# Performance work log

Hardware: AMD Instinct MI355X
Metric: run time of the kernel (lower is better)

Reference implementation:

```python
import jax, jax.numpy as jnp
import numpy as np

TEMPERATURE = 0.5
W_WITHIN = 1.0
W_CROSS = 0.5
MARGIN = 0.1


def setup_inputs() -> dict:
    key = jax.random.key(0)
    k1, k2 = jax.random.split(key)
    features = jax.random.normal(k1, (8192, 256), dtype=jnp.float32)
    gene_labels = jax.random.randint(k2, (8192,), 0, 200, dtype=jnp.int64 if jax.config.jax_enable_x64 else jnp.int32)
    return {"features": features, "gene_labels": gene_labels}


def reference(features, gene_labels):
    B = features.shape[0]
    # L2-normalize rows, full pairwise cosine similarity / temperature
    fn = features / jnp.linalg.norm(features, axis=1, keepdims=True)
    sim = (fn @ fn.T) / TEMPERATURE  # [B, B]

    same = gene_labels[:, None] == gene_labels[None, :]  # [B, B]
    eye = jnp.eye(B, dtype=bool)
    same_off = same & ~eye            # same-gene, off-diagonal (gene_similarity)
    neg = ~same                       # different-gene pairs (cross_gene_mask)
    has_neg = neg.any(axis=1)

    # Per-anchor logsumexp over negatives (sim of anchor i to all different-gene samples)
    neg_sim = jnp.where(neg, sim, -jnp.inf)
    lse_neg = jax.scipy.special.logsumexp(neg_sim, axis=1)
    lse_neg = jnp.where(has_neg, lse_neg, 0.0)  # rows with no negatives are masked out below

    # Within-gene loss: for each unordered same-gene pair (i<j) with gene != -1 and
    # anchor i having >=1 negative: CE([sim_ij, neg_sims_i], label=0)
    #   = -sim_ij + logaddexp(sim_ij, lse_neg_i) = softplus(lse_neg_i - sim_ij)
    upper = jnp.triu(jnp.ones((B, B), dtype=bool), k=1)
    valid_gene = (gene_labels != -1)[:, None]
    pair_mask = same_off & upper & valid_gene & has_neg[:, None]
    within_gene_loss = jnp.where(pair_mask, jax.nn.softplus(lse_neg[:, None] - sim), 0.0).sum()

    # Cross-gene loss: mean over all ordered different-gene pairs of relu(sim - margin)
    cross_cnt = neg.sum()
    cross_sum = jnp.where(neg, jax.nn.relu(sim - MARGIN), 0.0).sum()
    cross_gene_loss = jnp.where(cross_cnt > 0, cross_sum / jnp.maximum(cross_cnt, 1).astype(sim.dtype), 0.0)

    total_loss = W_WITHIN * within_gene_loss + W_CROSS * cross_gene_loss
    num_within_gene_pairs = same_off.sum().astype(sim.dtype)
    num_cross_gene_pairs = cross_cnt
    return total_loss, within_gene_loss, cross_gene_loss, num_within_gene_pairs, num_cross_gene_pairs
```

## Files before the change

kernel.cpp:

```cpp
#include <hip/hip_runtime.h>
#include <math.h>

#define B_N   8192
#define D_K   256
#define NGENE 200
#define MAXN  512

typedef short  bf16x8 __attribute__((ext_vector_type(8)));
typedef float  f32x4  __attribute__((ext_vector_type(4)));

#define OFF_FNBF    0u
#define OFF_LPART   4194304u
#define OFF_HIST    4718592u
#define OFF_OFFS    4719616u
#define OFF_SORTED  4720640u
#define OFF_CROSSP  4753408u
#define OFF_WITHINP 4755456u
#define OFF_CCORR   4756480u

__device__ __forceinline__ unsigned short f2bf(float f) {
    unsigned int u = __float_as_uint(f);
    unsigned int r = u + 0x7fffu + ((u >> 16) & 1u);
    return (unsigned short)(r >> 16);
}
__device__ __forceinline__ float bf2f_lo(unsigned int u) { return __uint_as_float(u << 16); }
__device__ __forceinline__ float bf2f_hi(unsigned int u) { return __uint_as_float(u & 0xffff0000u); }

__global__ __launch_bounds__(256) void k_np(const float* __restrict__ feat,
                                            const int* __restrict__ lab,
                                            unsigned short* __restrict__ fnbf,
                                            int* __restrict__ hist,
                                            int* __restrict__ offs,
                                            int* __restrict__ sorted) {
    if (blockIdx.x < 2048) {
        int wave = threadIdx.x >> 6, lane = threadIdx.x & 63;
        int row  = blockIdx.x * 4 + wave;
        const float4* src = reinterpret_cast<const float4*>(feat + (size_t)row * D_K);
        float4 v = src[lane];
        float ss = v.x * v.x + v.y * v.y + v.z * v.z + v.w * v.w;
#pragma unroll
        for (int m = 1; m < 64; m <<= 1) ss += __shfl_xor(ss, m);
        float rn = 1.0f / sqrtf(ss);
        ushort4 o;
        o.x = f2bf(v.x * rn); o.y = f2bf(v.y * rn);
        o.z = f2bf(v.z * rn); o.w = f2bf(v.w * rn);
        reinterpret_cast<ushort4*>(fnbf + (size_t)row * D_K)[lane] = o;
        return;
    }
    __shared__ int sh_hist[256], sh_scan[256], sh_cur[256];
    int t = threadIdx.x;
    sh_hist[t] = 0;
    __syncthreads();
    for (int i = t; i < B_N; i += 256) {
        int lb = lab[i];
        if (lb >= 0 && lb < NGENE) atomicAdd(&sh_hist[lb], 1);
    }
    __syncthreads();
    int v = sh_hist[t];
    sh_scan[t] = v;
    __syncthreads();
#pragma unroll
    for (int d = 1; d < 256; d <<= 1) {
        int x = (t >= d) ? sh_scan[t - d] : 0;
        __syncthreads();
        sh_scan[t] += x;
        __syncthreads();
    }
    int excl = sh_scan[t] - v;
    sh_cur[t] = excl;
    if (t < NGENE) { hist[t] = v; offs[t] = excl; }
    __syncthreads();
    for (int i = t; i < B_N; i += 256) {
        int lb = lab[i];
        if (lb >= 0 && lb < NGENE) {
            int pos = atomicAdd(&sh_cur[lb], 1);
            sorted[pos] = i;
        }
    }
}

#define GLOAD8(arr, vo) do {                                                                   \
    asm volatile("global_load_dwordx4 %0, %1, %2 offset:0"   : "=v"(arr[0]) : "v"(vo), "s"(fb)); \
    asm volatile("global_load_dwordx4 %0, %1, %2 offset:64"  : "=v"(arr[1]) : "v"(vo), "s"(fb)); \
    asm volatile("global_load_dwordx4 %0, %1, %2 offset:128" : "=v"(arr[2]) : "v"(vo), "s"(fb)); \
    asm volatile("global_load_dwordx4 %0, %1, %2 offset:192" : "=v"(arr[3]) : "v"(vo), "s"(fb)); \
    asm volatile("global_load_dwordx4 %0, %1, %2 offset:256" : "=v"(arr[4]) : "v"(vo), "s"(fb)); \
    asm volatile("global_load_dwordx4 %0, %1, %2 offset:320" : "=v"(arr[5]) : "v"(vo), "s"(fb)); \
    asm volatile("global_load_dwordx4 %0, %1, %2 offset:384" : "=v"(arr[6]) : "v"(vo), "s"(fb)); \
    asm volatile("global_load_dwordx4 %0, %1, %2 offset:448" : "=v"(arr[7]) : "v"(vo), "s"(fb)); \
} while (0)

#define GL_LDS16(gp, lp)                                                          \
    __builtin_amdgcn_global_load_lds(                                             \
        (const __attribute__((address_space(1))) unsigned int*)(gp),              \
        (__attribute__((address_space(3))) unsigned int*)(lp), 16, 0, 0)

#define Z4 ((f32x4){0.f, 0.f, 0.f, 0.f})
#define MFMA(A, B, C) __builtin_amdgcn_mfma_f32_16x16x32_bf16(A, B, C, 0, 0, 0)

#define EPI(AC, LS, CS) do {                                    \
    _Pragma("unroll")                                           \
    for (int r = 0; r < 4; ++r) {                               \
        float av = AC[r];                                       \
        LS[r] += __expf(2.0f * av);                             \
        CS += fmaxf(av - 0.05f, 0.f);                           \
    }                                                           \
} while (0)

#define STAGE(BUF) do {                    \
    GL_LDS16(g0, smem_c + (BUF) + st0);    \
    GL_LDS16(g1, smem_c + (BUF) + st1);    \
    GL_LDS16(g2, smem_c + (BUF) + st2);    \
    GL_LDS16(g3, smem_c + (BUF) + st3);    \
    g0 += 16384; g1 += 16384; g2 += 16384; g3 += 16384; \
} while (0)

#define WAIT_VM(n) do { asm volatile("s_waitcnt vmcnt(" #n ")" ::: "memory"); \
                        __builtin_amdgcn_sched_barrier(0); } while (0)

__global__ __launch_bounds__(256, 2) void k_pairwise(const unsigned short* __restrict__ fnbf,
                                                     float* __restrict__ l_part,
                                                     float* __restrict__ cross_part) {
    __shared__ __align__(16) char smem_c[65536];

    int wave = threadIdx.x >> 6, lane = threadIdx.x & 63;
    int g16 = lane >> 4, l16 = lane & 15;
    int l7 = l16 & 7;
    int rg = blockIdx.x, cwin = blockIdx.y;
    int r0 = rg * 256 + wave * 64;
    const unsigned short* fb = fnbf;

    bf16x8 a0[8], a1[8], a2[8], a3[8];
    unsigned voa = (unsigned)(r0 + l16) * 512u + (unsigned)g16 * 16u;
    GLOAD8(a0, voa); voa += 16u * 512u;
    GLOAD8(a1, voa); voa += 16u * 512u;
    GLOAD8(a2, voa); voa += 16u * 512u;
    GLOAD8(a3, voa);

    const char* gwin = (const char*)fnbf + (size_t)cwin * 262144u;
    const char *g0, *g1, *g2, *g3;
    {
        int f0 = wave * 256 + lane;
        int f1 = f0 + 64, f2 = f0 + 128, f3 = f0 + 192;
        int c0 = f0 >> 5, c1 = f1 >> 5, c2 = f2 >> 5, c3 = f3 >> 5;
        g0 = gwin + c0 * 512 + ((f0 & 31) ^ (c0 & 7)) * 16;
        g1 = gwin + c1 * 512 + ((f1 & 31) ^ (c1 & 7)) * 16;
        g2 = gwin + c2 * 512 + ((f2 & 31) ^ (c2 & 7)) * 16;
        g3 = gwin + c3 * 512 + ((f3 & 31) ^ (c3 & 7)) * 16;
    }
    unsigned st0 = wave * 4096u, st1 = st0 + 1024u,
             st2 = st0 + 2048u, st3 = st0 + 3072u;

    STAGE(0u);
    STAGE(16384u);
    STAGE(32768u);
    WAIT_VM(12);

    float lsum[4][4] = {};
    float cs0 = 0.f, cs1 = 0.f, cs2 = 0.f, cs3 = 0.f;
    int vb = l16 * 512;

#pragma unroll 1
    for (int st = 0; st < 16; ++st) {
        if (st < 14)      { WAIT_VM(8); }
        else if (st == 14){ WAIT_VM(4); }
        else              { WAIT_VM(0); }
        __builtin_amdgcn_s_barrier();

        if (st < 13) {
            unsigned nb = ((unsigned)(st + 3) & 3u) << 14;
            STAGE(nb);
        }

        const char* base = smem_c + (((unsigned)st & 3u) << 14);
        f32x4 acA0 = Z4, acA1 = Z4, acA2 = Z4, acA3 = Z4;
        f32x4 acB0 = Z4, acB1 = Z4, acB2 = Z4, acB3 = Z4;
#pragma unroll
        for (int ks = 0; ks < 8; ++ks) {
            const char* p = base + (unsigned)(vb + ((((ks << 2) | g16) ^ l7) << 4));
            bf16x8 bv0 = *(const bf16x8*)p;
            bf16x8 bv1 = *(const bf16x8*)(p + 8192);
            acA0 = MFMA(a0[ks], bv0, acA0);
            acA1 = MFMA(a1[ks], bv0, acA1);
            acA2 = MFMA(a2[ks], bv0, acA2);
            acA3 = MFMA(a3[ks], bv0, acA3);
            acB0 = MFMA(a0[ks], bv1, acB0);
            acB1 = MFMA(a1[ks], bv1, acB1);
            acB2 = MFMA(a2[ks], bv1, acB2);
            acB3 = MFMA(a3[ks], bv1, acB3);
        }
        EPI(acA0, lsum[0], cs0); EPI(acA1, lsum[1], cs1);
        EPI(acA2, lsum[2], cs2); EPI(acA3, lsum[3], cs3);
        EPI(acB0, lsum[0], cs0); EPI(acB1, lsum[1], cs1);
        EPI(acB2, lsum[2], cs2); EPI(acB3, lsum[3], cs3);
    }

#pragma unroll
    for (int t = 0; t < 4; ++t)
#pragma unroll
        for (int r = 0; r < 4; ++r) {
            float v = lsum[t][r];
            v += __shfl_xor(v, 1); v += __shfl_xor(v, 2);
            v += __shfl_xor(v, 4); v += __shfl_xor(v, 8);
            if (l16 == 0)
                l_part[(size_t)cwin * B_N + r0 + t * 16 + g16 * 4 + r] = v;
        }

    float c = (cs0 + cs1) + (cs2 + cs3);
#pragma unroll
    for (int m = 1; m < 64; m <<= 1) c += __shfl_xor(c, m);
    __shared__ float shc[4];
    if (lane == 0) shc[wave] = c;
    __syncthreads();
    if (threadIdx.x == 0)
        cross_part[cwin * 32 + rg] = shc[0] + shc[1] + shc[2] + shc[3];
}

__device__ __forceinline__ float dot_g(const uint4* __restrict__ fu, int i, int j) {
    const uint4* pa = fu + (size_t)i * 32;
    const uint4* pb = fu + (size_t)j * 32;
    float d = 0.f;
#pragma unroll
    for (int k = 0; k < 32; ++k) {
        uint4 ua = pa[k], ub = pb[k];
        d = fmaf(bf2f_lo(ua.x), bf2f_lo(ub.x), d);
        d = fmaf(bf2f_hi(ua.x), bf2f_hi(ub.x), d);
        d = fmaf(bf2f_lo(ua.y), bf2f_lo(ub.y), d);
        d = fmaf(bf2f_hi(ua.y), bf2f_hi(ub.y), d);
        d = fmaf(bf2f_lo(ua.z), bf2f_lo(ub.z), d);
        d = fmaf(bf2f_hi(ua.z), bf2f_hi(ub.z), d);
        d = fmaf(bf2f_lo(ua.w), bf2f_lo(ub.w), d);
        d = fmaf(bf2f_hi(ua.w), bf2f_hi(ub.w), d);
    }
    return d;
}

__global__ __launch_bounds__(256) void k_within(const unsigned short* __restrict__ fnbf,
                                                const int* __restrict__ hist,
                                                const int* __restrict__ offs,
                                                const int* __restrict__ sorted,
                                                const float* __restrict__ l_part,
                                                float* __restrict__ within_part,
                                                float* __restrict__ cross_corr) {
    int g = blockIdx.x;
    int n = hist[g], start = offs[g];
    int t = threadIdx.x;
    int wave = t >> 6, lane = t & 63;
    int g16 = lane >> 4, l16 = lane & 15;

    __shared__ float sim[128 * 130];
    __shared__ int   rid[MAXN];
    __shared__ float slse[MAXN];
    __shared__ float red[256];

    for (int idx = t; idx < n; idx += 256) rid[idx] = sorted[start + idx];
    __syncthreads();

    float ccor = 0.f, wsum = 0.f;

    if (n <= 128) {
        int NT = (n + 15) >> 4;
        const bf16x8* fv = reinterpret_cast<const bf16x8*>(fnbf);
        for (int tile = wave; tile < NT * NT; tile += 4) {
            int ti = tile / NT, tj = tile - ti * NT;
            int ia = ti * 16 + l16;
            int ib = tj * 16 + l16;
            int ra = rid[ia < n ? ia : (n - 1)];
            int rb = rid[ib < n ? ib : (n - 1)];
            f32x4 acc = Z4;
#pragma unroll
            for (int ks = 0; ks < 8; ++ks) {
                bf16x8 av = fv[(size_t)ra * 32 + ks * 4 + g16];
                bf16x8 bv = fv[(size_t)rb * 32 + ks * 4 + g16];
                acc = MFMA(av, bv, acc);
            }
            int si = ti * 16 + g16 * 4;
            int sj = tj * 16 + l16;
#pragma unroll
            for (int r = 0; r < 4; ++r)
                sim[(si + r) * 130 + sj] = acc[r];
        }
        __syncthreads();

        for (int i = t; i < n; i += 256) {
            float raw = 0.f;
#pragma unroll
            for (int k = 0; k < 16; ++k) raw += l_part[(size_t)k * B_N + rid[i]];
            const float* srow = &sim[i * 130];
            float esum = 0.f;
            for (int j = 0; j < n; ++j) {
                float s = 2.0f * srow[j];
                esum += __expf(s);
                ccor += fmaxf(s - 0.1f, 0.f);
            }
            slse[i] = __logf(raw - esum);
        }
        __syncthreads();

        int nn = n * n;
        for (int p = t; p < nn; p += 256) {
            int i = p / n, j = p - i * n;
            if (j <= i) continue;
            float s = 2.0f * sim[i * 130 + j];
            int ai = (rid[i] < rid[j]) ? i : j;
            float x = slse[ai] - s;
            wsum += fmaxf(x, 0.f) + log1pf(__expf(-fabsf(x)));
        }
    } else {
        const uint4* fu = reinterpret_cast<const uint4*>(fnbf);
        for (int i = t; i < n; i += 256) {
            float raw = 0.f;
#pragma unroll
            for (int k = 0; k < 16; ++k) raw += l_part[(size_t)k * B_N + rid[i]];
            float esum = 0.f;
            for (int j = 0; j < n; ++j) {
                float s = 2.0f * dot_g(fu, rid[i], rid[j]);
                esum += __expf(s);
                ccor += fmaxf(s - 0.1f, 0.f);
            }
            slse[i] = __logf(raw - esum);
        }
        __syncthreads();
        int nn = n * n;
        for (int p = t; p < nn; p += 256) {
            int i = p / n, j = p - i * n;
            if (j <= i) continue;
            float s = 2.0f * dot_g(fu, rid[i], rid[j]);
            int ai = (rid[i] < rid[j]) ? i : j;
            float x = slse[ai] - s;
            wsum += fmaxf(x, 0.f) + log1pf(__expf(-fabsf(x)));
        }
    }

    red[t] = wsum;
    __syncthreads();
#pragma unroll
    for (int d2 = 128; d2 > 0; d2 >>= 1) {
        if (t < d2) red[t] += red[t + d2];
        __syncthreads();
    }
    if (t == 0) within_part[g] = red[0];
    __syncthreads();
    red[t] = ccor;
    __syncthreads();
#pragma unroll
    for (int d2 = 128; d2 > 0; d2 >>= 1) {
        if (t < d2) red[t] += red[t + d2];
        __syncthreads();
    }
    if (t == 0) cross_corr[g] = red[0];
}

__global__ __launch_bounds__(256) void k_finalize(const float* __restrict__ cross_part,
                                                  const float* __restrict__ within_part,
                                                  const float* __restrict__ cross_corr,
                                                  const int* __restrict__ hist,
                                                  float* __restrict__ out) {
    __shared__ float shc[256];
    __shared__ float shw[256];
    __shared__ float shk[256];
    __shared__ long long shs[256];
    int t = threadIdx.x;
    float cs = 0.f;
    for (int i = t; i < 512; i += 256) cs += cross_part[i];
    float wv = 0.f, cc = 0.f;
    long long s2 = 0;
    if (t < NGENE) {
        wv = within_part[t];
        cc = cross_corr[t];
        long long h = hist[t];
        s2 = h * h;
    }
    shc[t] = cs; shw[t] = wv; shk[t] = cc; shs[t] = s2;
    __syncthreads();
#pragma unroll
    for (int d = 128; d > 0; d >>= 1) {
        if (t < d) {
            shc[t] += shc[t + d]; shw[t] += shw[t + d];
            shk[t] += shk[t + d]; shs[t] += shs[t + d];
        }
        __syncthreads();
    }
    if (t == 0) {
        long long S  = shs[0];
        long long nw = S - (long long)B_N;
        long long nc = (long long)B_N * (long long)B_N - S;
        float cross_total = 2.0f * shc[0] - shk[0];
        float cross_loss = (nc > 0) ? (cross_total / (float)(nc > 1 ? nc : 1)) : 0.f;
        float within     = shw[0];
        out[0] = within + 0.5f * cross_loss;
        out[1] = within;
        out[2] = cross_loss;
        out[3] = (float)nw;
        out[4] = (float)nc;
    }
}

extern "C" void kernel_launch(void* const* d_in, const int* in_sizes, int n_in,
                              void* d_out, int out_size, void* d_ws, size_t ws_size,
                              hipStream_t stream) {
    const float* feat = (const float*)d_in[0];
    const int*   lab  = (const int*)d_in[1];
    float* out = (float*)d_out;
    char* ws = (char*)d_ws;

    unsigned short* fnbf = (unsigned short*)(ws + OFF_FNBF);
    float* l_part        = (float*)(ws + OFF_LPART);
    int*   hist          = (int*)(ws + OFF_HIST);
    int*   offs          = (int*)(ws + OFF_OFFS);
    int*   sorted        = (int*)(ws + OFF_SORTED);
    float* cross_part    = (float*)(ws + OFF_CROSSP);
    float* within_part   = (float*)(ws + OFF_WITHINP);
    float* cross_corr    = (float*)(ws + OFF_CCORR);

    k_np<<<2049, 256, 0, stream>>>(feat, lab, fnbf, hist, offs, sorted);
    k_pairwise<<<dim3(32, 16), 256, 0, stream>>>(fnbf, l_part, cross_part);
    k_within<<<NGENE, 256, 0, stream>>>(fnbf, hist, offs, sorted, l_part, within_part, cross_corr);
    k_finalize<<<1, 256, 0, stream>>>(cross_part, within_part, cross_corr, hist, out);
}
```

Before: 94.23 us.

## Shrink pairwise blocks to 128 rows, double-buffer LDS, swizzle block order

The pairwise GEMM kernel now uses 128-thread blocks covering 128 rows each, giving 1024 blocks instead of 512. LDS staging drops from a 4-deep ring to a 2-deep double buffer (32KB), which allows more blocks per CU. A 1D grid with a block-index swizzle groups blocks that share column windows for better L2 reuse. In exchange, each staged column tile is reused by only two waves, so operand loads per MFMA rise, and the prefetch depth is shallower with a full vmcnt(0) wait every step.

```diff
diff --git a/kernel.cpp b/kernel.cpp
--- a/kernel.cpp
+++ b/kernel.cpp
@@ -15,8 +15,8 @@
 #define OFF_OFFS    4719616u
 #define OFF_SORTED  4720640u
 #define OFF_CROSSP  4753408u
-#define OFF_WITHINP 4755456u
-#define OFF_CCORR   4756480u
+#define OFF_WITHINP 4757504u
+#define OFF_CCORR   4758528u
 
 __device__ __forceinline__ unsigned short f2bf(float f) {
     unsigned int u = __float_as_uint(f);
@@ -107,27 +107,32 @@
     }                                                           \
 } while (0)
 
-#define STAGE(BUF) do {                    \
-    GL_LDS16(g0, smem_c + (BUF) + st0);    \
-    GL_LDS16(g1, smem_c + (BUF) + st1);    \
-    GL_LDS16(g2, smem_c + (BUF) + st2);    \
-    GL_LDS16(g3, smem_c + (BUF) + st3);    \
-    g0 += 16384; g1 += 16384; g2 += 16384; g3 += 16384; \
-} while (0)
-
 #define WAIT_VM(n) do { asm volatile("s_waitcnt vmcnt(" #n ")" ::: "memory"); \
                         __builtin_amdgcn_sched_barrier(0); } while (0)
 
-__global__ __launch_bounds__(256, 2) void k_pairwise(const unsigned short* __restrict__ fnbf,
+#define STAGE8(BUF, ST) do {                                                       \
+    const char* gsb = gw + (unsigned)(ST) * 16384u;                                \
+    _Pragma("unroll")                                                              \
+    for (int q = 0; q < 8; ++q)                                                    \
+        GL_LDS16(gsb + sv[q], smem_c + (BUF) + sd[q]);                             \
+} while (0)
+
+__global__ __launch_bounds__(128, 2) void k_pairwise(const unsigned short* __restrict__ fnbf,
                                                      float* __restrict__ l_part,
                                                      float* __restrict__ cross_part) {
-    __shared__ __align__(16) char smem_c[65536];
-
-    int wave = threadIdx.x >> 6, lane = threadIdx.x & 63;
+    __shared__ __align__(16) char smem_c[32768];
+    __shared__ float shc[2];
+
+    int tid = threadIdx.x;
+    int wave = tid >> 6, lane = tid & 63;
     int g16 = lane >> 4, l16 = lane & 15;
     int l7 = l16 & 7;
-    int rg = blockIdx.x, cwin = blockIdx.y;
-    int r0 = rg * 256 + wave * 64;
+
+    int b = blockIdx.x;
+    int swz = (b & 7) * 128 + (b >> 3);
+    int rg = swz & 63, cwin = swz >> 6;
+
+    int r0 = rg * 128 + wave * 64;
     const unsigned short* fb = fnbf;
 
     bf16x8 a0[8], a1[8], a2[8], a3[8];
@@ -137,24 +142,18 @@
     GLOAD8(a2, voa); voa += 16u * 512u;
     GLOAD8(a3, voa);
 
-    const char* gwin = (const char*)fnbf + (size_t)cwin * 262144u;
-    const char *g0, *g1, *g2, *g3;
-    {
-        int f0 = wave * 256 + lane;
-        int f1 = f0 + 64, f2 = f0 + 128, f3 = f0 + 192;
-        int c0 = f0 >> 5, c1 = f1 >> 5, c2 = f2 >> 5, c3 = f3 >> 5;
-        g0 = gwin + c0 * 512 + ((f0 & 31) ^ (c0 & 7)) * 16;
-        g1 = gwin + c1 * 512 + ((f1 & 31) ^ (c1 & 7)) * 16;
-        g2 = gwin + c2 * 512 + ((f2 & 31) ^ (c2 & 7)) * 16;
-        g3 = gwin + c3 * 512 + ((f3 & 31) ^ (c3 & 7)) * 16;
-    }
-    unsigned st0 = wave * 4096u, st1 = st0 + 1024u,
-             st2 = st0 + 2048u, st3 = st0 + 3072u;
-
-    STAGE(0u);
-    STAGE(16384u);
-    STAGE(32768u);
-    WAIT_VM(12);
+    const char* gw = (const char*)fnbf + (size_t)cwin * 262144u;
+    unsigned sv[8], sd[8];
+#pragma unroll
+    for (int q = 0; q < 8; ++q) {
+        int f = q * 128 + tid;
+        int col = f >> 5;
+        sv[q] = (unsigned)(col * 512 + (((tid & 31) ^ (col & 7)) << 4));
+        sd[q] = (unsigned)(f << 4);
+    }
+
+    STAGE8(0u, 0);
+    WAIT_VM(8);
 
     float lsum[4][4] = {};
     float cs0 = 0.f, cs1 = 0.f, cs2 = 0.f, cs3 = 0.f;
@@ -162,17 +161,11 @@
 
 #pragma unroll 1
     for (int st = 0; st < 16; ++st) {
-        if (st < 14)      { WAIT_VM(8); }
-        else if (st == 14){ WAIT_VM(4); }
-        else              { WAIT_VM(0); }
+        WAIT_VM(0);
         __builtin_amdgcn_s_barrier();
-
-        if (st < 13) {
-            unsigned nb = ((unsigned)(st + 3) & 3u) << 14;
-            STAGE(nb);
-        }
-
-        const char* base = smem_c + (((unsigned)st & 3u) << 14);
+        if (st < 15) STAGE8((unsigned)(((st + 1) & 1) << 14), st + 1);
+
+        const char* base = smem_c + ((st & 1) << 14);
         f32x4 acA0 = Z4, acA1 = Z4, acA2 = Z4, acA3 = Z4;
         f32x4 acB0 = Z4, acB1 = Z4, acB2 = Z4, acB3 = Z4;
 #pragma unroll
@@ -209,11 +202,10 @@
     float c = (cs0 + cs1) + (cs2 + cs3);
 #pragma unroll
     for (int m = 1; m < 64; m <<= 1) c += __shfl_xor(c, m);
-    __shared__ float shc[4];
     if (lane == 0) shc[wave] = c;
     __syncthreads();
-    if (threadIdx.x == 0)
-        cross_part[cwin * 32 + rg] = shc[0] + shc[1] + shc[2] + shc[3];
+    if (tid == 0)
+        cross_part[cwin * 64 + rg] = shc[0] + shc[1];
 }
 
 __device__ __forceinline__ float dot_g(const uint4* __restrict__ fu, int i, int j) {
@@ -362,7 +354,7 @@
     __shared__ long long shs[256];
     int t = threadIdx.x;
     float cs = 0.f;
-    for (int i = t; i < 512; i += 256) cs += cross_part[i];
+    for (int i = t; i < 1024; i += 256) cs += cross_part[i];
     float wv = 0.f, cc = 0.f;
     long long s2 = 0;
     if (t < NGENE) {
@@ -414,7 +406,7 @@
     float* cross_corr    = (float*)(ws + OFF_CCORR);
 
     k_np<<<2049, 256, 0, stream>>>(feat, lab, fnbf, hist, offs, sorted);
-    k_pairwise<<<dim3(32, 16), 256, 0, stream>>>(fnbf, l_part, cross_part);
+    k_pairwise<<<1024, 128, 0, stream>>>(fnbf, l_part, cross_part);
     k_within<<<NGENE, 256, 0, stream>>>(fnbf, hist, offs, sorted, l_part, within_part, cross_corr);
     k_finalize<<<1, 256, 0, stream>>>(cross_part, within_part, cross_corr, hist, out);
 }
```

After: 116.6 us. 23.7% more time.
